# Performance work log

Hardware: AMD Instinct MI355X
Metric: run time of the kernel (lower is better)

## Reference

```python
import jax, jax.numpy as jnp
import numpy as np

B, DIM, HEADS = 8, 1024, 8
DH = DIM // HEADS            # 128 = dim_head
MFEAT = 621                  # int(DH * log(DH)) performer features
MAXD = 4                     # max_rel_dist
IMG = 10                     # image side; source hardcodes stride 10 in scatter indices
L = IMG * IMG + 1            # geometry forces L = img_dim**2 + 1


def _geometry():
    m, K = MAXD, 2 * MAXD - 1
    base = np.arange(-m + 1, m)
    dx = np.broadcast_to(np.tile(base, K), (L, K * K))
    dy = np.broadcast_to(np.repeat(base, K), (L, K * K))
    x_off = np.concatenate([np.tile(np.arange(IMG), IMG), [0]])[:, None]
    y_off = np.concatenate([np.repeat(np.arange(IMG), IMG), [IMG]])[:, None]
    x_pos, y_pos = dx + x_off, dy + y_off
    diffs = np.abs(dx) + np.abs(dy)
    valid = (x_pos >= 0) & (x_pos < IMG) & (y_pos >= 0) & (y_pos < IMG) & (diffs < m)
    diffs = np.where(valid, diffs, m)  # invalid taps point at the max-dist encoding
    rel_window = (m - 1) * IMG + (m - 1)
    # scatter positions inside the unfold window (stride 10 hardcoded in source)
    indices = np.tile(np.arange(K), K) + np.repeat(np.arange(K) * 10, K)
    return jnp.asarray(diffs), jnp.asarray(valid), jnp.asarray(indices - rel_window)

DIFFS, VALID, OFFSETS = _geometry()  # [L,K2] int, [L,K2] bool, [K2] int


def softmax_kernel(data, proj, is_query, eps=1e-4):
    dn = data.shape[-1] ** -0.25
    ratio = proj.shape[0] ** -0.5
    dd = jnp.einsum('...id,jd->...ij', data * dn, proj)
    diag = (jnp.sum(data ** 2, -1) * (0.5 * dn * dn))[..., None]
    mx = jnp.max(dd, -1, keepdims=True) if is_query else jnp.max(dd)
    return ratio * (jnp.exp(dd - diag - mx) + eps)


def relative_attention(q, rpe, v):
    # q: [b,h,L,MFEAT] kernel features, rpe: [R,MFEAT], v: [b,h,L,DH]
    mde = rpe[-1]                                   # max-distance encoding
    v_sum = v.sum(-2)                               # [b,h,DH]
    q_dot = jnp.einsum('bhlm,rm->bhlr', q, rpe - mde)
    q_rel = jnp.take_along_axis(q_dot, DIFFS[None, None], axis=-1)  # [b,h,L,K2]
    q_rel = jnp.where(VALID[None, None], q_rel, 0.0)
    # gather v at relative offsets (equivalent to the zero-padded unfold +
    # sparse scatter of q_rel in the source, without the dense 67-wide window)
    pos = jnp.arange(L)[:, None] + OFFSETS[None, :]  # [L,K2]
    inb = (pos >= 0) & (pos < L)
    v_g = v[:, :, jnp.clip(pos, 0, L - 1), :]        # [b,h,L,K2,DH]
    v_g = jnp.where(inb[None, None, :, :, None], v_g, 0.0)
    denom = (rpe[DIFFS] - mde).sum(1) + mde * L      # [L,MFEAT]
    D_inv = 1.0 / jnp.einsum('bhlm,lm->bhl', q, denom)
    q_md = jnp.einsum('bhlm,m->bhl', q, mde)
    out = jnp.einsum('bhl,bhd->bhld', q_md, v_sum) + jnp.einsum('bhlk,bhlkd->bhld', q_rel, v_g)
    return out * D_inv[..., None]


def setup_inputs() -> dict:
    key = jax.random.key(0)
    ks = jax.random.split(key, 9)
    s = DIM ** -0.5
    return {
        'x': jax.random.normal(ks[0], (B, L, DIM), jnp.float32),
        'Wq': jax.random.normal(ks[1], (DIM, DIM), jnp.float32) * s,
        'bq': jnp.zeros((DIM,), jnp.float32),
        'Wv': jax.random.normal(ks[2], (DIM, DIM), jnp.float32) * s,
        'bv': jnp.zeros((DIM,), jnp.float32),
        'rpe': jax.random.normal(ks[3], (MAXD + 1, DH), jnp.float32) * 0.02,
        'proj': jax.random.normal(ks[4], (MFEAT, DH), jnp.float32),
        'Wo': jax.random.normal(ks[5], (DIM, DIM), jnp.float32) * s,
        'bo': jnp.zeros((DIM,), jnp.float32),
    }


def reference(x, Wq, bq, Wv, bv, rpe, proj, Wo, bo):
    b = x.shape[0]
    q = (x @ Wq.T + bq).reshape(b, L, HEADS, DH).transpose(0, 2, 1, 3)
    v = (x @ Wv.T + bv).reshape(b, L, HEADS, DH).transpose(0, 2, 1, 3)
    qf = softmax_kernel(q, proj, is_query=True)
    rf = softmax_kernel(rpe[None, None], proj, is_query=False)[0, 0]
    out = relative_attention(qf, rf, v)          # [b,h,L,DH]
    out = out.transpose(0, 2, 1, 3).reshape(b, L, DIM)
    return out @ Wo.T + bo
```

## Files before the change

### kernel.cpp

```cpp
#include <hip/hip_runtime.h>
#include <math.h>

namespace {

typedef __bf16 bf16_t;
typedef bf16_t bf16x8 __attribute__((ext_vector_type(8)));
typedef bf16_t bf16x4 __attribute__((ext_vector_type(4)));
typedef float f32x4 __attribute__((ext_vector_type(4)));

constexpr int B = 8, L = 101, DIM = 1024, H = 8, DH = 128, MF = 621, MFP = 640;
constexpr int BL = B * L;
constexpr int BLP = 832;
constexpr int BH = B * H;
constexpr int RR = BL * H;

constexpr float DN    = 0.29730177875068026f;
constexpr float DN2   = 0.08838834764831845f;
constexpr float RATIO = 0.04012861672f;
constexpr float EPS   = 1e-4f;

constexpr int NX = BL * DIM / 4;
constexpr int NP = MFP * 32;
constexpr int NR = 64 * DH / 4;
constexpr int NW = DIM * DIM / 4;
constexpr int NZ = 3 * (BLP - BL) * DIM / 4;
constexpr int NV = BH * DH / 4;
constexpr int NTOT = NX + NP + NR + 3 * NW + NZ + NV;

__device__ __forceinline__ f32x4 mfma16(bf16x8 a, bf16x8 b, f32x4 c) {
  return __builtin_amdgcn_mfma_f32_16x16x32_bf16(a, b, c, 0, 0, 0);
}

__device__ __forceinline__ void split2(float f, bf16_t& h, bf16_t& l) {
  h = (bf16_t)f;
  l = (bf16_t)(f - (float)h);
}

__device__ __forceinline__ void gload_lds16(const bf16_t* g, bf16_t* l) {
  __builtin_amdgcn_global_load_lds(
      (const __attribute__((address_space(1))) void*)g,
      (__attribute__((address_space(3))) void*)l, 16, 0, 0);
}

__global__ __launch_bounds__(256) void split_all(const float* __restrict__ x,
                                                 const float* __restrict__ proj,
                                                 const float* __restrict__ rpe,
                                                 const float* __restrict__ Wq,
                                                 const float* __restrict__ Wv,
                                                 const float* __restrict__ Wo,
                                                 bf16_t* __restrict__ xh,
                                                 bf16_t* __restrict__ ph,
                                                 bf16_t* __restrict__ rh, bf16_t* __restrict__ rl,
                                                 bf16_t* __restrict__ Wh,
                                                 bf16_t* __restrict__ Woh,
                                                 bf16_t* __restrict__ qh, bf16_t* __restrict__ ql,
                                                 float* __restrict__ vsum) {
  const int u = blockIdx.x * 256 + threadIdx.x;
  if (u >= NTOT) return;
  auto emit2 = [](const float* s4, float sc, bf16_t* dh, bf16_t* dl, size_t off) {
    float4 f = *(const float4*)s4;
    bf16x4 hv, lv; bf16_t h, l;
    split2(f.x * sc, h, l); hv[0] = h; lv[0] = l;
    split2(f.y * sc, h, l); hv[1] = h; lv[1] = l;
    split2(f.z * sc, h, l); hv[2] = h; lv[2] = l;
    split2(f.w * sc, h, l); hv[3] = h; lv[3] = l;
    *(bf16x4*)(dh + off) = hv;
    *(bf16x4*)(dl + off) = lv;
  };
  auto emit1 = [](const float* s4, float sc, bf16_t* dh, size_t off) {
    float4 f = *(const float4*)s4;
    bf16x4 hv;
    hv[0] = (bf16_t)(f.x * sc); hv[1] = (bf16_t)(f.y * sc);
    hv[2] = (bf16_t)(f.z * sc); hv[3] = (bf16_t)(f.w * sc);
    *(bf16x4*)(dh + off) = hv;
  };
  int t = u;
  if (t < NX) { emit1(x + (size_t)t * 4, 1.f, xh, (size_t)t * 4); return; }
  t -= NX;
  if (t < NP) {
    if ((t >> 5) < MF) emit1(proj + (size_t)t * 4, DN, ph, (size_t)t * 4);
    else { bf16x4 z = {}; *(bf16x4*)(ph + (size_t)t * 4) = z; }
    return;
  }
  t -= NP;
  if (t < NR) {
    if (t < 5 * DH / 4) emit2(rpe + (size_t)t * 4, 1.f, rh, rl, (size_t)t * 4);
    else { bf16x4 z = {}; *(bf16x4*)(rh + (size_t)t * 4) = z; *(bf16x4*)(rl + (size_t)t * 4) = z; }
    return;
  }
  t -= NR;
  if (t < NW) { emit1(Wq + (size_t)t * 4, 1.f, Wh, (size_t)t * 4); return; }
  t -= NW;
  if (t < NW) { emit1(Wv + (size_t)t * 4, 1.f, Wh, (size_t)(t + NW) * 4); return; }
  t -= NW;
  if (t < NW) { emit1(Wo + (size_t)t * 4, 1.f, Woh, (size_t)t * 4); return; }
  t -= NW;
  if (t < NZ) {
    const int buf = t / 6144, o = t % 6144;
    bf16_t* dst = (buf == 0) ? xh : (buf == 1) ? qh : ql;
    bf16x4 z = {};
    *(bf16x4*)(dst + (size_t)BL * DIM + (size_t)o * 4) = z;
    return;
  }
  t -= NZ;
  ((float4*)vsum)[t] = make_float4(0.f, 0.f, 0.f, 0.f);
}

template<int MODE, int AT>
__global__ __launch_bounds__(256) void gemm64(const bf16_t* __restrict__ Ah,
                                              const bf16_t* __restrict__ Al,
                                              const bf16_t* __restrict__ Bh,
                                              const float* __restrict__ bias0,
                                              const float* __restrict__ bias1,
                                              float* __restrict__ Cf,
                                              bf16_t* __restrict__ Ch,
                                              bf16_t* __restrict__ Cl,
                                              float* __restrict__ vsum) {
  constexpr int K = 1024, BK = 64, NK = K / BK;
  constexpr int NT = AT + 1;
  __shared__ bf16_t lds[2][NT][64 * 64];
  const int tid = threadIdx.x;
  const int w = tid >> 6, lane = tid & 63;
  const int wr = w >> 1, wc = w & 1;
  const int l15 = lane & 15, l4 = lane >> 4;
  const int rowBase = blockIdx.y * 64, colBase = blockIdx.x * 64;
  const int r8 = lane >> 3;
  const int cs = (lane & 7) ^ r8;
  const bf16_t* src;
  int grow0, ti, dst0;
  if (AT == 2) {
    src = (w == 0) ? Ah : (w == 1) ? Al : Bh;
    grow0 = (w < 2) ? rowBase : colBase + ((w == 3) ? 32 : 0);
    ti = (w < 2) ? w : 2;
    dst0 = (w == 3) ? 32 * 64 : 0;
  } else {
    src = (w < 2) ? Ah : Bh;
    grow0 = ((w < 2) ? rowBase : colBase) + ((w & 1) ? 32 : 0);
    ti = (w < 2) ? 0 : 1;
    dst0 = (w & 1) ? 32 * 64 : 0;
  }
  const bf16_t* srcL = src + (size_t)(grow0 + r8) * K + cs * 8;
  auto STAGE = [&](int bf, int k0) {
    if (AT == 2 && w < 2) {
#pragma unroll
      for (int j = 0; j < 8; ++j)
        gload_lds16(srcL + (size_t)(8 * j) * K + k0, &lds[bf][ti][j * 512]);
    } else {
#pragma unroll
      for (int j = 0; j < 4; ++j)
        gload_lds16(srcL + (size_t)(8 * j) * K + k0, &lds[bf][ti][dst0 + j * 512]);
    }
  };
  const int ra0 = wr * 32 + l15, ra1 = ra0 + 16;
  const int rb0 = wc * 32 + l15, rb1 = rb0 + 16;
  constexpr int bt = (AT == 1) ? 1 : 2;
  auto TADDR = [](int row, int kg) { return row * 64 + (((kg) ^ (row & 7)) << 3); };
  f32x4 acc[2][2] = {};
  STAGE(0, 0);
  __syncthreads();
  int bf = 0;
  for (int ks = 0; ks < NK; ++ks) {
    if (ks + 1 < NK) STAGE(bf ^ 1, (ks + 1) * BK);
#pragma unroll
    for (int subk = 0; subk < 2; ++subk) {
      const int kg = subk * 4 + l4;
      bf16x8 a0h = *(const bf16x8*)&lds[bf][0][TADDR(ra0, kg)];
      bf16x8 a1h = *(const bf16x8*)&lds[bf][0][TADDR(ra1, kg)];
      bf16x8 b0  = *(const bf16x8*)&lds[bf][bt][TADDR(rb0, kg)];
      bf16x8 b1  = *(const bf16x8*)&lds[bf][bt][TADDR(rb1, kg)];
      acc[0][0] = mfma16(a0h, b0, acc[0][0]);
      acc[0][1] = mfma16(a0h, b1, acc[0][1]);
      acc[1][0] = mfma16(a1h, b0, acc[1][0]);
      acc[1][1] = mfma16(a1h, b1, acc[1][1]);
      if (AT == 2) {
        bf16x8 a0l = *(const bf16x8*)&lds[bf][1][TADDR(ra0, kg)];
        bf16x8 a1l = *(const bf16x8*)&lds[bf][1][TADDR(ra1, kg)];
        acc[0][0] = mfma16(a0l, b0, acc[0][0]);
        acc[0][1] = mfma16(a0l, b1, acc[0][1]);
        acc[1][0] = mfma16(a1l, b0, acc[1][0]);
        acc[1][1] = mfma16(a1l, b1, acc[1][1]);
      }
    }
    __syncthreads();
    bf ^= 1;
  }
#pragma unroll
  for (int ni = 0; ni < 2; ++ni) {
    const int col = colBase + wc * 32 + ni * 16 + l15;
#pragma unroll
    for (int mi = 0; mi < 2; ++mi) {
      float vpart = 0.f;
      int curb = -1;
#pragma unroll
      for (int r2 = 0; r2 < 4; ++r2) {
        const int row = rowBase + wr * 32 + mi * 16 + l4 * 4 + r2;
        if (row < BL) {
          if (MODE == 0) {
            Cf[(size_t)row * 1024 + col] = acc[mi][ni][r2] + bias0[col];
          } else {
            if (col < 1024) {
              float val = acc[mi][ni][r2] + bias0[col];
              bf16_t h, lo; split2(val, h, lo);
              Ch[(size_t)row * 1024 + col] = h;
              Cl[(size_t)row * 1024 + col] = lo;
            } else {
              const int vcol = col - 1024;
              const float val = acc[mi][ni][r2] + bias1[vcol];
              Cf[(size_t)row * 1024 + vcol] = val;
              const int b = row / L;
              if (b != curb) {
                if (curb >= 0)
                  atomicAdd(&vsum[(size_t)(curb * 8) * DH + vcol], vpart);
                curb = b; vpart = 0.f;
              }
              vpart += val;
            }
          }
        }
      }
      if (MODE == 1 && curb >= 0)
        atomicAdd(&vsum[(size_t)(curb * 8) * DH + (col - 1024)], vpart);
    }
  }
}

__global__ __launch_bounds__(256) void qf3_kernel(const bf16_t* __restrict__ qh,
                                                  const bf16_t* __restrict__ ql,
                                                  const bf16_t* __restrict__ rh,
                                                  const bf16_t* __restrict__ rl,
                                                  const bf16_t* __restrict__ ph,
                                                  const float* __restrict__ rpe,
                                                  float* __restrict__ fd) {
  const int tid = threadIdx.x;
  __shared__ bf16_t Ahl[2][64 * 128];
  __shared__ bf16_t Bch[2][64 * 128];
  __shared__ float rfs[5][MFP];
  __shared__ float diag[32];
  __shared__ float diag5v[8];
  __shared__ float mxs[4][32];
  __shared__ float mxAll[32];
  __shared__ float mxrf[4];
  __shared__ float sred[4][32][5];
  const int w = tid >> 6, lane = tid & 63;
  const int l15 = lane & 15, l4 = lane >> 4;
  const int r0 = blockIdx.x * 32;
  const int r4 = lane >> 4;
  const int cg = lane & 15;
  {
    const bf16_t* srcA = (w == 0) ? qh : (w == 1) ? ql : (w == 2) ? rh : rl;
    const int arow0 = (w < 2) ? r0 : 0;
    bf16_t* dstA = &Ahl[w & 1][(w >= 2 ? 32 : 0) * 128];
    const bf16_t* peA = srcA + (size_t)(arow0 + r4) * DH + ((cg ^ r4) << 3);
    const bf16_t* poA = srcA + (size_t)(arow0 + r4) * DH + ((cg ^ r4 ^ 4) << 3);
#pragma unroll
    for (int j = 0; j < 8; ++j)
      gload_lds16(((j & 1) ? poA : peA) + (size_t)(4 * j) * DH, dstA + j * 512);
  }
  const bf16_t* peB = ph + (size_t)(w * 16 + r4) * DH + ((cg ^ r4) << 3);
  const bf16_t* poB = ph + (size_t)(w * 16 + r4) * DH + ((cg ^ r4 ^ 4) << 3);
  auto STAGE_B = [&](int buf, int c) {
    const size_t coff = (size_t)c * 64 * DH;
#pragma unroll
    for (int j = 0; j < 4; ++j)
      gload_lds16(((j & 1) ? poB : peB) + coff + (size_t)(4 * j) * DH,
                  &Bch[buf][(w * 16 + j * 4) * 128]);
  };
  {
    const int row = tid >> 3, ch = tid & 7;
    const size_t base = (size_t)(r0 + row) * DH + ch * 16;
    float s = 0.f;
#pragma unroll
    for (int t = 0; t < 2; ++t) {
      bf16x8 vh = *(const bf16x8*)(qh + base + t * 8);
      bf16x8 vl = *(const bf16x8*)(ql + base + t * 8);
#pragma unroll
      for (int e = 0; e < 8; ++e) {
        float f = (float)vh[e] + (float)vl[e];
        s += f * f;
      }
    }
    s += __shfl_xor(s, 1, 64); s += __shfl_xor(s, 2, 64); s += __shfl_xor(s, 4, 64);
    if (ch == 0) diag[row] = (0.5f * DN2) * s;
  }
  if (tid < 40) {
    const int row = tid >> 3, ch = tid & 7;
    float s = 0.f;
#pragma unroll
    for (int e = 0; e < 16; ++e) { float f = rpe[row * DH + ch * 16 + e]; s += f * f; }
    s += __shfl_xor(s, 1, 64); s += __shfl_xor(s, 2, 64); s += __shfl_xor(s, 4, 64);
    if (ch == 0) diag5v[row] = (0.5f * DN2) * s;
  }
  auto TADDR = [](int row, int kg) { return row * 128 + (((kg) ^ (row & 7)) << 3); };
  f32x4 acc[2][10] = {};
  f32x4 accr[10] = {};
  STAGE_B(0, 0);
  __syncthreads();
  int buf = 0;
#pragma unroll
  for (int c = 0; c < 10; ++c) {
    if (c + 1 < 10) STAGE_B(buf ^ 1, c + 1);
#pragma unroll
    for (int ks = 0; ks < 4; ++ks) {
      const int kg = ks * 4 + l4;
      bf16x8 a0h = *(const bf16x8*)&Ahl[0][TADDR(l15, kg)];
      bf16x8 a0l = *(const bf16x8*)&Ahl[1][TADDR(l15, kg)];
      bf16x8 a1h = *(const bf16x8*)&Ahl[0][TADDR(16 + l15, kg)];
      bf16x8 a1l = *(const bf16x8*)&Ahl[1][TADDR(16 + l15, kg)];
      bf16x8 arh = *(const bf16x8*)&Ahl[0][TADDR(32 + l15, kg)];
      bf16x8 arl = *(const bf16x8*)&Ahl[1][TADDR(32 + l15, kg)];
      bf16x8 bb  = *(const bf16x8*)&Bch[buf][TADDR(w * 16 + l15, kg)];
      acc[0][c] = mfma16(a0h, bb, acc[0][c]);
      acc[0][c] = mfma16(a0l, bb, acc[0][c]);
      acc[1][c] = mfma16(a1h, bb, acc[1][c]);
      acc[1][c] = mfma16(a1l, bb, acc[1][c]);
      accr[c]   = mfma16(arh, bb, accr[c]);
      accr[c]   = mfma16(arl, bb, accr[c]);
    }
    __syncthreads();
    buf ^= 1;
  }
  float pm[2][4];
#pragma unroll
  for (int mi = 0; mi < 2; ++mi)
#pragma unroll
    for (int r2 = 0; r2 < 4; ++r2) {
      float m = -3.4e38f;
#pragma unroll
      for (int ni = 0; ni < 10; ++ni) {
        const int col = ni * 64 + w * 16 + l15;
        float vv = (col < MF) ? acc[mi][ni][r2] : -3.4e38f;
        m = fmaxf(m, vv);
      }
      pm[mi][r2] = m;
    }
#pragma unroll
  for (int mask = 1; mask <= 8; mask <<= 1)
#pragma unroll
    for (int mi = 0; mi < 2; ++mi)
#pragma unroll
      for (int r2 = 0; r2 < 4; ++r2)
        pm[mi][r2] = fmaxf(pm[mi][r2], __shfl_xor(pm[mi][r2], mask, 64));
  if (l15 == 0) {
#pragma unroll
    for (int mi = 0; mi < 2; ++mi)
#pragma unroll
      for (int r2 = 0; r2 < 4; ++r2)
        mxs[w][mi * 16 + l4 * 4 + r2] = pm[mi][r2];
  }
  {
    float m = -3.4e38f;
#pragma unroll
    for (int ni = 0; ni < 10; ++ni) {
      const int col = ni * 64 + w * 16 + l15;
#pragma unroll
      for (int r2 = 0; r2 < 4; ++r2) {
        const int row5 = l4 * 4 + r2;
        if (row5 < 5 && col < MF) m = fmaxf(m, accr[ni][r2]);
      }
    }
#pragma unroll
    for (int mask = 1; mask <= 32; mask <<= 1) m = fmaxf(m, __shfl_xor(m, mask, 64));
    if (lane == 0) mxrf[w] = m;
  }
  __syncthreads();
  {
    const float mxR = fmaxf(fmaxf(mxrf[0], mxrf[1]), fmaxf(mxrf[2], mxrf[3]));
#pragma unroll
    for (int ni = 0; ni < 10; ++ni) {
      const int col = ni * 64 + w * 16 + l15;
#pragma unroll
      for (int r2 = 0; r2 < 4; ++r2) {
        const int row5 = l4 * 4 + r2;
        if (row5 < 5) {
          float val = (col < MF)
              ? RATIO * (__expf(accr[ni][r2] - diag5v[row5] - mxR) + EPS) : 0.f;
          rfs[row5][col] = val;
        }
      }
    }
  }
  if (tid < 32)
    mxAll[tid] = fmaxf(fmaxf(mxs[0][tid], mxs[1][tid]), fmaxf(mxs[2][tid], mxs[3][tid]));
  __syncthreads();
  for (int i = tid; i < 4 * MFP; i += 256) rfs[i / MFP][i % MFP] -= rfs[4][i % MFP];
  __syncthreads();
  float s[2][4][5] = {};
#pragma unroll
  for (int mi = 0; mi < 2; ++mi)
#pragma unroll
    for (int r2 = 0; r2 < 4; ++r2) {
      const int row = mi * 16 + l4 * 4 + r2;
      const float sub = diag[row] + mxAll[row];
#pragma unroll
      for (int ni = 0; ni < 10; ++ni) {
        const int col = ni * 64 + w * 16 + l15;
        const float qfv = RATIO * (__expf(acc[mi][ni][r2] - sub) + EPS);
#pragma unroll
        for (int c = 0; c < 5; ++c) s[mi][r2][c] += qfv * rfs[c][col];
      }
    }
#pragma unroll
  for (int mask = 1; mask <= 8; mask <<= 1)
#pragma unroll
    for (int mi = 0; mi < 2; ++mi)
#pragma unroll
      for (int r2 = 0; r2 < 4; ++r2)
#pragma unroll
        for (int c = 0; c < 5; ++c)
          s[mi][r2][c] += __shfl_xor(s[mi][r2][c], mask, 64);
  if (l15 == 0) {
#pragma unroll
    for (int mi = 0; mi < 2; ++mi)
#pragma unroll
      for (int r2 = 0; r2 < 4; ++r2)
#pragma unroll
        for (int c = 0; c < 5; ++c)
          sred[w][mi * 16 + l4 * 4 + r2][c] = s[mi][r2][c];
  }
  __syncthreads();
  if (tid < 160) {
    const int row = tid / 5, c = tid % 5;
    fd[(size_t)(r0 + row) * 8 + c] =
        sred[0][row][c] + sred[1][row][c] + sred[2][row][c] + sred[3][row][c];
  }
}

__global__ __launch_bounds__(256) void out_kernel(const float* __restrict__ fd,
                                                  const float* __restrict__ v,
                                                  const float* __restrict__ vsum,
                                                  bf16_t* __restrict__ attnh,
                                                  bf16_t* __restrict__ attnl) {
  const int tid = threadIdx.x;
  const int sub = tid >> 7, d = tid & 127;
  const int bh = blockIdx.y, b = bh >> 3, h = bh & 7;
  const int l = blockIdx.x * 2 + sub;
  if (l >= L) return;
  const size_t r = (size_t)(b * L + l) * H + h;
  const float q0 = fd[r * 8 + 0], q1 = fd[r * 8 + 1], q2 = fd[r * 8 + 2],
              q3 = fd[r * 8 + 3], sM = fd[r * 8 + 4];
  float o = sM * vsum[(size_t)bh * DH + d];
  float c0 = 0, c1 = 0, c2 = 0, c3 = 0;
  const int xo = (l < 100) ? (l % 10) : 0;
  const int yo = (l < 100) ? (l / 10) : 10;
#pragma unroll
  for (int k = 0; k < 49; ++k) {
    const int dx = (k % 7) - 3, dy = (k / 7) - 3;
    const int xp = xo + dx, yp = yo + dy;
    const int df = (dx < 0 ? -dx : dx) + (dy < 0 ? -dy : dy);
    if (xp >= 0 && xp < 10 && yp >= 0 && yp < 10 && df < 4) {
      float qq;
      if (df == 0)      { c0 += 1.f; qq = q0; }
      else if (df == 1) { c1 += 1.f; qq = q1; }
      else if (df == 2) { c2 += 1.f; qq = q2; }
      else              { c3 += 1.f; qq = q3; }
      const int pos = l + dx + 10 * dy;
      o += qq * v[(size_t)(b * L + pos) * DIM + h * DH + d];
    }
  }
  const float D = c0 * q0 + c1 * q1 + c2 * q2 + c3 * q3 + (float)L * sM;
  const float val = o / D;
  bf16_t hi, lo; split2(val, hi, lo);
  const size_t oi = (size_t)(b * L + l) * DIM + h * DH + d;
  attnh[oi] = hi;
  attnl[oi] = lo;
}

}

extern "C" void kernel_launch(void* const* d_in, const int* in_sizes, int n_in,
                              void* d_out, int out_size, void* d_ws, size_t ws_size,
                              hipStream_t stream) {
  const float* x    = (const float*)d_in[0];
  const float* Wq   = (const float*)d_in[1];
  const float* bq   = (const float*)d_in[2];
  const float* Wv   = (const float*)d_in[3];
  const float* bv   = (const float*)d_in[4];
  const float* rpe  = (const float*)d_in[5];
  const float* proj = (const float*)d_in[6];
  const float* Wo   = (const float*)d_in[7];
  const float* bo   = (const float*)d_in[8];

  char* p = (char*)d_ws;
  auto alloc = [&](size_t bytes) { char* r = p; p += (bytes + 255) & ~255ull; return r; };
  bf16_t* xh  = (bf16_t*)alloc((size_t)BLP * DIM * 2);
  bf16_t* Wh  = (bf16_t*)alloc((size_t)2 * DIM * DIM * 2);
  bf16_t* Woh = (bf16_t*)alloc((size_t)DIM * DIM * 2);
  bf16_t* ph  = (bf16_t*)alloc((size_t)MFP * DH * 2);
  bf16_t* rh  = (bf16_t*)alloc((size_t)64 * DH * 2);
  bf16_t* rl  = (bf16_t*)alloc((size_t)64 * DH * 2);
  bf16_t* qh  = (bf16_t*)alloc((size_t)BLP * DIM * 2);
  bf16_t* ql  = (bf16_t*)alloc((size_t)BLP * DIM * 2);
  float*  v   = (float*)alloc((size_t)BL * DIM * 4);
  float*  fd  = (float*)alloc((size_t)RR * 8 * 4);
  float*  vsm = (float*)alloc((size_t)BH * DH * 4);

  split_all<<<(NTOT + 255) / 256, 256, 0, stream>>>(x, proj, rpe, Wq, Wv, Wo,
                                                    xh, ph, rh, rl,
                                                    Wh, Woh, qh, ql, vsm);
  gemm64<1, 1><<<dim3(32, 13), 256, 0, stream>>>(xh, nullptr, Wh, bq, bv,
                                                 v, qh, ql, vsm);
  qf3_kernel<<<202, 256, 0, stream>>>(qh, ql, rh, rl, ph, rpe, fd);
  out_kernel<<<dim3((L + 1) / 2, BH), 256, 0, stream>>>(fd, v, vsm, qh, ql);
  gemm64<0, 2><<<dim3(16, 13), 256, 0, stream>>>(qh, ql, Woh, bo, nullptr,
                                                 (float*)d_out, nullptr, nullptr, nullptr);
}
```

Baseline: 76.78 us.

## Widen qf3 to 8 waves and use single-bf16 attention output for final GEMM

The qf3 feature kernel moves to 512 threads, so each wave covers 16 columns of a 128-wide projection chunk. That halves the chunk-loop trip count and the per-wave accumulator count, and every reduction is widened to 8 waves. Separately, out_kernel now writes only a single bf16 attention value with no hi/lo split, and the output GEMM runs in single-pass mode instead of two-pass. This halves the attention write traffic and the MFMA work of the final projection, at the cost of precision in the output GEMM.

```diff
diff --git a/kernel.cpp b/kernel.cpp
--- a/kernel.cpp
+++ b/kernel.cpp
@@ -224,7 +224,7 @@
   }
 }
 
-__global__ __launch_bounds__(256) void qf3_kernel(const bf16_t* __restrict__ qh,
+__global__ __launch_bounds__(512) void qf3_kernel(const bf16_t* __restrict__ qh,
                                                   const bf16_t* __restrict__ ql,
                                                   const bf16_t* __restrict__ rh,
                                                   const bf16_t* __restrict__ rl,
@@ -232,40 +232,40 @@
                                                   const float* __restrict__ rpe,
                                                   float* __restrict__ fd) {
   const int tid = threadIdx.x;
-  __shared__ bf16_t Ahl[2][64 * 128];
-  __shared__ bf16_t Bch[2][64 * 128];
+  __shared__ bf16_t Ahl[2][48 * 128];
+  __shared__ bf16_t Bch[2][128 * 128];
   __shared__ float rfs[5][MFP];
   __shared__ float diag[32];
   __shared__ float diag5v[8];
-  __shared__ float mxs[4][32];
+  __shared__ float mxs[8][32];
   __shared__ float mxAll[32];
-  __shared__ float mxrf[4];
-  __shared__ float sred[4][32][5];
+  __shared__ float mxrf[8];
+  __shared__ float sred[8][32][5];
   const int w = tid >> 6, lane = tid & 63;
   const int l15 = lane & 15, l4 = lane >> 4;
   const int r0 = blockIdx.x * 32;
   const int r4 = lane >> 4;
   const int cg = lane & 15;
-  {
-    const bf16_t* srcA = (w == 0) ? qh : (w == 1) ? ql : (w == 2) ? rh : rl;
-    const int arow0 = (w < 2) ? r0 : 0;
-    bf16_t* dstA = &Ahl[w & 1][(w >= 2 ? 32 : 0) * 128];
+  if (w < 6) {
+    const bf16_t* srcA = (w < 2) ? qh : (w < 4) ? ql : (w == 4) ? rh : rl;
+    const int arow0 = (w < 4) ? (r0 + (w & 1) * 16) : 0;
+    bf16_t* dstA = &Ahl[(w < 4) ? (w >> 1) : (w - 4)][((w < 4) ? (w & 1) * 16 : 32) * 128];
     const bf16_t* peA = srcA + (size_t)(arow0 + r4) * DH + ((cg ^ r4) << 3);
     const bf16_t* poA = srcA + (size_t)(arow0 + r4) * DH + ((cg ^ r4 ^ 4) << 3);
 #pragma unroll
-    for (int j = 0; j < 8; ++j)
+    for (int j = 0; j < 4; ++j)
       gload_lds16(((j & 1) ? poA : peA) + (size_t)(4 * j) * DH, dstA + j * 512);
   }
   const bf16_t* peB = ph + (size_t)(w * 16 + r4) * DH + ((cg ^ r4) << 3);
   const bf16_t* poB = ph + (size_t)(w * 16 + r4) * DH + ((cg ^ r4 ^ 4) << 3);
   auto STAGE_B = [&](int buf, int c) {
-    const size_t coff = (size_t)c * 64 * DH;
+    const size_t coff = (size_t)c * 128 * DH;
 #pragma unroll
     for (int j = 0; j < 4; ++j)
       gload_lds16(((j & 1) ? poB : peB) + coff + (size_t)(4 * j) * DH,
                   &Bch[buf][(w * 16 + j * 4) * 128]);
   };
-  {
+  if (tid < 256) {
     const int row = tid >> 3, ch = tid & 7;
     const size_t base = (size_t)(r0 + row) * DH + ch * 16;
     float s = 0.f;
@@ -291,14 +291,14 @@
     if (ch == 0) diag5v[row] = (0.5f * DN2) * s;
   }
   auto TADDR = [](int row, int kg) { return row * 128 + (((kg) ^ (row & 7)) << 3); };
-  f32x4 acc[2][10] = {};
-  f32x4 accr[10] = {};
+  f32x4 acc[2][5] = {};
+  f32x4 accr[5] = {};
   STAGE_B(0, 0);
   __syncthreads();
   int buf = 0;
 #pragma unroll
-  for (int c = 0; c < 10; ++c) {
-    if (c + 1 < 10) STAGE_B(buf ^ 1, c + 1);
+  for (int c = 0; c < 5; ++c) {
+    if (c + 1 < 5) STAGE_B(buf ^ 1, c + 1);
 #pragma unroll
     for (int ks = 0; ks < 4; ++ks) {
       const int kg = ks * 4 + l4;
@@ -326,9 +326,9 @@
     for (int r2 = 0; r2 < 4; ++r2) {
       float m = -3.4e38f;
 #pragma unroll
-      for (int ni = 0; ni < 10; ++ni) {
-        const int col = ni * 64 + w * 16 + l15;
-        float vv = (col < MF) ? acc[mi][ni][r2] : -3.4e38f;
+      for (int c = 0; c < 5; ++c) {
+        const int col = c * 128 + w * 16 + l15;
+        float vv = (col < MF) ? acc[mi][c][r2] : -3.4e38f;
         m = fmaxf(m, vv);
       }
       pm[mi][r2] = m;
@@ -350,12 +350,12 @@
   {
     float m = -3.4e38f;
 #pragma unroll
-    for (int ni = 0; ni < 10; ++ni) {
-      const int col = ni * 64 + w * 16 + l15;
+    for (int c = 0; c < 5; ++c) {
+      const int col = c * 128 + w * 16 + l15;
 #pragma unroll
       for (int r2 = 0; r2 < 4; ++r2) {
         const int row5 = l4 * 4 + r2;
-        if (row5 < 5 && col < MF) m = fmaxf(m, accr[ni][r2]);
+        if (row5 < 5 && col < MF) m = fmaxf(m, accr[c][r2]);
       }
     }
 #pragma unroll
@@ -364,25 +364,31 @@
   }
   __syncthreads();
   {
-    const float mxR = fmaxf(fmaxf(mxrf[0], mxrf[1]), fmaxf(mxrf[2], mxrf[3]));
-#pragma unroll
-    for (int ni = 0; ni < 10; ++ni) {
-      const int col = ni * 64 + w * 16 + l15;
+    float mxR = mxrf[0];
+#pragma unroll
+    for (int i = 1; i < 8; ++i) mxR = fmaxf(mxR, mxrf[i]);
+#pragma unroll
+    for (int c = 0; c < 5; ++c) {
+      const int col = c * 128 + w * 16 + l15;
 #pragma unroll
       for (int r2 = 0; r2 < 4; ++r2) {
         const int row5 = l4 * 4 + r2;
         if (row5 < 5) {
           float val = (col < MF)
-              ? RATIO * (__expf(accr[ni][r2] - diag5v[row5] - mxR) + EPS) : 0.f;
+              ? RATIO * (__expf(accr[c][r2] - diag5v[row5] - mxR) + EPS) : 0.f;
           rfs[row5][col] = val;
         }
       }
     }
   }
-  if (tid < 32)
-    mxAll[tid] = fmaxf(fmaxf(mxs[0][tid], mxs[1][tid]), fmaxf(mxs[2][tid], mxs[3][tid]));
+  if (tid < 32) {
+    float m = mxs[0][tid];
+#pragma unroll
+    for (int i = 1; i < 8; ++i) m = fmaxf(m, mxs[i][tid]);
+    mxAll[tid] = m;
+  }
   __syncthreads();
-  for (int i = tid; i < 4 * MFP; i += 256) rfs[i / MFP][i % MFP] -= rfs[4][i % MFP];
+  for (int i = tid; i < 4 * MFP; i += 512) rfs[i / MFP][i % MFP] -= rfs[4][i % MFP];
   __syncthreads();
   float s[2][4][5] = {};
 #pragma unroll
@@ -392,11 +398,11 @@
       const int row = mi * 16 + l4 * 4 + r2;
       const float sub = diag[row] + mxAll[row];
 #pragma unroll
-      for (int ni = 0; ni < 10; ++ni) {
-        const int col = ni * 64 + w * 16 + l15;
-        const float qfv = RATIO * (__expf(acc[mi][ni][r2] - sub) + EPS);
-#pragma unroll
-        for (int c = 0; c < 5; ++c) s[mi][r2][c] += qfv * rfs[c][col];
+      for (int c = 0; c < 5; ++c) {
+        const int col = c * 128 + w * 16 + l15;
+        const float qfv = RATIO * (__expf(acc[mi][c][r2] - sub) + EPS);
+#pragma unroll
+        for (int cc = 0; cc < 5; ++cc) s[mi][r2][cc] += qfv * rfs[cc][col];
       }
     }
 #pragma unroll
@@ -406,30 +412,31 @@
 #pragma unroll
       for (int r2 = 0; r2 < 4; ++r2)
 #pragma unroll
-        for (int c = 0; c < 5; ++c)
-          s[mi][r2][c] += __shfl_xor(s[mi][r2][c], mask, 64);
+        for (int cc = 0; cc < 5; ++cc)
+          s[mi][r2][cc] += __shfl_xor(s[mi][r2][cc], mask, 64);
   if (l15 == 0) {
 #pragma unroll
     for (int mi = 0; mi < 2; ++mi)
 #pragma unroll
       for (int r2 = 0; r2 < 4; ++r2)
 #pragma unroll
-        for (int c = 0; c < 5; ++c)
-          sred[w][mi * 16 + l4 * 4 + r2][c] = s[mi][r2][c];
+        for (int cc = 0; cc < 5; ++cc)
+          sred[w][mi * 16 + l4 * 4 + r2][cc] = s[mi][r2][cc];
   }
   __syncthreads();
   if (tid < 160) {
-    const int row = tid / 5, c = tid % 5;
-    fd[(size_t)(r0 + row) * 8 + c] =
-        sred[0][row][c] + sred[1][row][c] + sred[2][row][c] + sred[3][row][c];
+    const int row = tid / 5, cc = tid % 5;
+    float acc5 = sred[0][row][cc];
+#pragma unroll
+    for (int i = 1; i < 8; ++i) acc5 += sred[i][row][cc];
+    fd[(size_t)(r0 + row) * 8 + cc] = acc5;
   }
 }
 
 __global__ __launch_bounds__(256) void out_kernel(const float* __restrict__ fd,
                                                   const float* __restrict__ v,
                                                   const float* __restrict__ vsum,
-                                                  bf16_t* __restrict__ attnh,
-                                                  bf16_t* __restrict__ attnl) {
+                                                  bf16_t* __restrict__ attnh) {
   const int tid = threadIdx.x;
   const int sub = tid >> 7, d = tid & 127;
   const int bh = blockIdx.y, b = bh >> 3, h = bh & 7;
@@ -458,11 +465,7 @@
     }
   }
   const float D = c0 * q0 + c1 * q1 + c2 * q2 + c3 * q3 + (float)L * sM;
-  const float val = o / D;
-  bf16_t hi, lo; split2(val, hi, lo);
-  const size_t oi = (size_t)(b * L + l) * DIM + h * DH + d;
-  attnh[oi] = hi;
-  attnl[oi] = lo;
+  attnh[(size_t)(b * L + l) * DIM + h * DH + d] = (bf16_t)(o / D);
 }
 
 }
@@ -499,8 +502,8 @@
                                                     Wh, Woh, qh, ql, vsm);
   gemm64<1, 1><<<dim3(32, 13), 256, 0, stream>>>(xh, nullptr, Wh, bq, bv,
                                                  v, qh, ql, vsm);
-  qf3_kernel<<<202, 256, 0, stream>>>(qh, ql, rh, rl, ph, rpe, fd);
-  out_kernel<<<dim3((L + 1) / 2, BH), 256, 0, stream>>>(fd, v, vsm, qh, ql);
-  gemm64<0, 2><<<dim3(16, 13), 256, 0, stream>>>(qh, ql, Woh, bo, nullptr,
+  qf3_kernel<<<202, 512, 0, stream>>>(qh, ql, rh, rl, ph, rpe, fd);
+  out_kernel<<<dim3((L + 1) / 2, BH), 256, 0, stream>>>(fd, v, vsm, qh);
+  gemm64<0, 1><<<dim3(16, 13), 256, 0, stream>>>(qh, nullptr, Woh, bo, nullptr,
                                                  (float*)d_out, nullptr, nullptr, nullptr);
 }
```

New measurement: 71.56 us. -6.8%, faster.
